# Optimization experiments

Measured on AMD Instinct MI355X. Metric: run time of the kernel, lower is better.

Reference implementation:

```python
import jax, jax.numpy as jnp
import numpy as np

N_NODES = 100000
N_EDGES = 3200000


def gcn_conv(x, edge_index, W, b, num_nodes):
    """PyG GCNConv: x' = D^{-1/2} (A + I) D^{-1/2} (x W) + b (symmetric norm, self-loops)."""
    x = x @ W  # [N, out]
    loop = jnp.arange(num_nodes, dtype=edge_index.dtype)
    src = jnp.concatenate([edge_index[0], loop])
    dst = jnp.concatenate([edge_index[1], loop])
    # degree over destination nodes (incl. self loops)
    deg = jax.ops.segment_sum(jnp.ones_like(dst, dtype=x.dtype), dst, num_segments=num_nodes)
    dinv = jnp.where(deg > 0, jax.lax.rsqrt(deg), 0.0)
    norm = dinv[src] * dinv[dst]  # [E + N]
    msg = x[src] * norm[:, None]  # gather + scale
    out = jax.ops.segment_sum(msg, dst, num_segments=num_nodes)  # scatter-add
    return out + b


def setup_inputs() -> dict:
    key = jax.random.key(0)
    k = jax.random.split(key, 5)
    x = jax.random.normal(k[0], (N_NODES, 256), dtype=jnp.float32)
    edge_index = jax.random.randint(k[1], (2, N_EDGES), 0, N_NODES, dtype=jnp.int64)
    W1 = jax.random.normal(k[2], (256, 16), dtype=jnp.float32) * (1.0 / np.sqrt(256))
    b1 = jnp.zeros((16,), dtype=jnp.float32)
    W2 = jax.random.normal(k[3], (16, 8), dtype=jnp.float32) * (1.0 / np.sqrt(16))
    b2 = jnp.zeros((8,), dtype=jnp.float32)
    return {"x": x, "edge_index": edge_index, "W1": W1, "b1": b1, "W2": W2, "b2": b2}


def reference(x, edge_index, W1, b1, W2, b2):
    n = x.shape[0]
    h = gcn_conv(x, edge_index, W1, b1, n)
    h = jax.nn.relu(h)
    # dropout is identity in eval mode (training=False)
    h = gcn_conv(h, edge_index, W2, b2, n)
    return jax.nn.log_softmax(h, axis=1)
```

## Files before the change

kernel.cpp:

```cpp
#include <hip/hip_runtime.h>

#define NN 100000
#define NE 3200000
#define NB 391
#define CAP 9216
#define PB 16
#define CH_A (256 * PB)
#define BIN_NBLK ((NE + CH_A - 1) / CH_A)
#define GEMM_NBLK (NN / 32)
#define FXS 65536.0f
#define FXI (1.0f / 65536.0f)

typedef _Float16 half4 __attribute__((ext_vector_type(4)));
typedef _Float16 half8 __attribute__((ext_vector_type(8)));

__device__ __forceinline__ float4 f4fma(float s, float4 a, float4 c) {
  c.x = fmaf(s, a.x, c.x); c.y = fmaf(s, a.y, c.y);
  c.z = fmaf(s, a.z, c.z); c.w = fmaf(s, a.w, c.w);
  return c;
}

template<int CTRL>
__device__ __forceinline__ float4 quad_bcast(float4 v) {
  float4 r;
  r.x = __int_as_float(__builtin_amdgcn_update_dpp(__float_as_int(v.x), __float_as_int(v.x), CTRL, 0xF, 0xF, false));
  r.y = __int_as_float(__builtin_amdgcn_update_dpp(__float_as_int(v.y), __float_as_int(v.y), CTRL, 0xF, 0xF, false));
  r.z = __int_as_float(__builtin_amdgcn_update_dpp(__float_as_int(v.z), __float_as_int(v.z), CTRL, 0xF, 0xF, false));
  r.w = __int_as_float(__builtin_amdgcn_update_dpp(__float_as_int(v.w), __float_as_int(v.w), CTRL, 0xF, 0xF, false));
  return r;
}

__global__ __launch_bounds__(256) void k1_kernel(const int* __restrict__ ei,
                                                 int* __restrict__ bucket_cursor,
                                                 int* __restrict__ pairs,
                                                 const float* __restrict__ x,
                                                 const float* __restrict__ W1,
                                                 _Float16* __restrict__ xw1h) {
  int t = threadIdx.x;
  if (blockIdx.x < BIN_NBLK) {
    __shared__ int  cnt[4][NB];
    __shared__ int  wcur[4][NB];
    __shared__ int  lbase[NB];
    __shared__ int  gbase[NB];
    __shared__ int  sc[512];
    __shared__ int2 stage[CH_A];
    __shared__ int  w64flag;
    int wv = t >> 6;
    for (int k = t; k < 4 * NB; k += 256) (&cnt[0][0])[k] = 0;
    if (t < 64) {
      int o = (t < 32) ? ei[2 * t + 1] : 0;
      unsigned long long bl = __ballot(o != 0);
      if (t == 0) w64flag = (bl == 0ULL) ? 1 : 0;
    }
    __syncthreads();
    bool w64 = (w64flag != 0);
    int base = blockIdx.x * CH_A;
    int nval = min(CH_A, NE - base);
    int s[PB], d[PB];
    if (w64) {
#pragma unroll
      for (int i = 0; i < 8; ++i) {
        int e0 = base + i * 512 + 2 * t;
        if (e0 < NE) {
          int4 svv = *(const int4*)(ei + 2 * (size_t)e0);
          int4 dvv = *(const int4*)(ei + 2 * (size_t)NE + 2 * (size_t)e0);
          s[2 * i] = svv.x; s[2 * i + 1] = svv.z;
          d[2 * i] = dvv.x; d[2 * i + 1] = dvv.z;
          atomicAdd(&cnt[wv][dvv.x >> 8], 1);
          atomicAdd(&cnt[wv][dvv.z >> 8], 1);
        } else {
          d[2 * i] = -1; d[2 * i + 1] = -1;
        }
      }
    } else {
#pragma unroll
      for (int i = 0; i < PB; ++i) {
        int e = base + i * 256 + t;
        if (e < NE) {
          s[i] = ei[e];
          d[i] = ei[NE + e];
          atomicAdd(&cnt[wv][d[i] >> 8], 1);
        } else {
          d[i] = -1;
        }
      }
    }
    __syncthreads();
    int tA = (t < NB) ? cnt[0][t] + cnt[1][t] + cnt[2][t] + cnt[3][t] : 0;
    int tB = (t + 256 < NB) ? cnt[0][t + 256] + cnt[1][t + 256] + cnt[2][t + 256] + cnt[3][t + 256] : 0;
    sc[t] = tA; sc[t + 256] = tB;
    __syncthreads();
#pragma unroll
    for (int off = 1; off < 512; off <<= 1) {
      int u0 = (t >= off) ? sc[t - off] : 0;
      int u1 = (t + 256 >= off) ? sc[t + 256 - off] : 0;
      __syncthreads();
      sc[t] += u0; sc[t + 256] += u1;
      __syncthreads();
    }
#pragma unroll
    for (int h = 0; h < 2; ++h) {
      int k = t + h * 256;
      if (k < NB) {
        int tot = (h == 0) ? tA : tB;
        int lb = sc[k] - tot;
        lbase[k] = lb;
        gbase[k] = (tot > 0) ? atomicAdd(&bucket_cursor[k], tot) : 0;
        int c0 = cnt[0][k], c1 = cnt[1][k], c2 = cnt[2][k];
        wcur[0][k] = lb;
        wcur[1][k] = lb + c0;
        wcur[2][k] = lb + c0 + c1;
        wcur[3][k] = lb + c0 + c1 + c2;
      }
    }
    __syncthreads();
#pragma unroll
    for (int i = 0; i < PB; ++i) {
      if (d[i] >= 0) {
        int b = d[i] >> 8;
        int slot = atomicAdd(&wcur[wv][b], 1);
        stage[slot] = make_int2(s[i], d[i]);
      }
    }
    __syncthreads();
    for (int k = t; k < nval; k += 256) {
      int2 p = stage[k];
      int b = p.y >> 8;
      pairs[(size_t)b * CAP + gbase[b] + (k - lbase[b])] = p.x | ((p.y & 255) << 24);
    }
  } else {
    const int bid  = blockIdx.x - BIN_NBLK;
    const int lane = t & 63;
    const int wv   = t >> 6;
    const int node0 = (bid * 4 + wv) * 8;
    const int cg = lane >> 2;
    const int jl = lane & 3;
    float4 w[16];
#pragma unroll
    for (int k = 0; k < 4; ++k)
#pragma unroll
      for (int c = 0; c < 4; ++c)
        w[k * 4 + c] = *(const float4*)(W1 + (cg * 16 + k * 4 + c) * 16 + jl * 4);
    float4 xv[8];
#pragma unroll
    for (int i = 0; i < 8; ++i)
      xv[i] = *(const float4*)(x + (size_t)(node0 + i) * 256 + lane * 4);
    float4 acc[8];
#pragma unroll
    for (int i = 0; i < 8; ++i) acc[i] = make_float4(0.f, 0.f, 0.f, 0.f);
#pragma unroll
    for (int i = 0; i < 8; ++i) {
      float4 b = quad_bcast<0x00>(xv[i]);
      acc[i] = f4fma(b.x, w[0], acc[i]);  acc[i] = f4fma(b.y, w[1], acc[i]);
      acc[i] = f4fma(b.z, w[2], acc[i]);  acc[i] = f4fma(b.w, w[3], acc[i]);
    }
#pragma unroll
    for (int i = 0; i < 8; ++i) {
      float4 b = quad_bcast<0x55>(xv[i]);
      acc[i] = f4fma(b.x, w[4], acc[i]);  acc[i] = f4fma(b.y, w[5], acc[i]);
      acc[i] = f4fma(b.z, w[6], acc[i]);  acc[i] = f4fma(b.w, w[7], acc[i]);
    }
#pragma unroll
    for (int i = 0; i < 8; ++i) {
      float4 b = quad_bcast<0xAA>(xv[i]);
      acc[i] = f4fma(b.x, w[8], acc[i]);  acc[i] = f4fma(b.y, w[9], acc[i]);
      acc[i] = f4fma(b.z, w[10], acc[i]); acc[i] = f4fma(b.w, w[11], acc[i]);
    }
#pragma unroll
    for (int i = 0; i < 8; ++i) {
      float4 b = quad_bcast<0xFF>(xv[i]);
      acc[i] = f4fma(b.x, w[12], acc[i]); acc[i] = f4fma(b.y, w[13], acc[i]);
      acc[i] = f4fma(b.z, w[14], acc[i]); acc[i] = f4fma(b.w, w[15], acc[i]);
    }
#pragma unroll
    for (int m = 4; m <= 32; m <<= 1) {
#pragma unroll
      for (int i = 0; i < 8; ++i) {
        acc[i].x += __shfl_xor(acc[i].x, m);
        acc[i].y += __shfl_xor(acc[i].y, m);
        acc[i].z += __shfl_xor(acc[i].z, m);
        acc[i].w += __shfl_xor(acc[i].w, m);
      }
    }
    if (lane < 4) {
#pragma unroll
      for (int i = 0; i < 8; ++i) {
        float4 a = acc[i];
        half4 hv;
        hv[0] = (_Float16)a.x; hv[1] = (_Float16)a.y;
        hv[2] = (_Float16)a.z; hv[3] = (_Float16)a.w;
        *(half4*)(xw1h + (size_t)(node0 + i) * 16 + lane * 4) = hv;
      }
    }
  }
}

__global__ __launch_bounds__(512) void hist_kernel(const int* __restrict__ pairs,
                                                   const int* __restrict__ bucket_cursor,
                                                   float* __restrict__ dinv) {
  __shared__ int hist[2][256];
  int t = threadIdx.x;
  int b = blockIdx.x;
  int cnt_b = bucket_cursor[b];
  size_t in_base = (size_t)b * CAP;
  if (t < 256) { hist[0][t] = 0; hist[1][t] = 0; }
  __syncthreads();
  int hs = t >> 8;
  for (int i = t; i < cnt_b; i += 512) {
    int pk = pairs[in_base + i];
    atomicAdd(&hist[hs][((unsigned)pk) >> 24], 1);
  }
  __syncthreads();
  if (t < 256) {
    int n = b * 256 + t;
    if (n < NN)
      dinv[n] = rsqrtf((float)(hist[0][t] + hist[1][t]) + 1.0f);
  }
}

__global__ __launch_bounds__(1024) void agg1_kernel(const int* __restrict__ pairs,
                                                    const int* __restrict__ bucket_cursor,
                                                    const float* __restrict__ dinv,
                                                    const _Float16* __restrict__ xw1h,
                                                    const float* __restrict__ W2,
                                                    const float* __restrict__ b1,
                                                    _Float16* __restrict__ h1w2h) {
  __shared__ int acc[16][257];
  int t = threadIdx.x;
  int b = blockIdx.x;
  int cnt_b = bucket_cursor[b];
  size_t in_base = (size_t)b * CAP;
  for (int k = t; k < 16 * 257; k += 1024) (&acc[0][0])[k] = 0;
  __syncthreads();
  for (int i = t; i < cnt_b; i += 1024) {
    int pk = pairs[in_base + i];
    int s  = pk & 0xFFFFFF;
    int nl = ((unsigned)pk) >> 24;
    float dvs = dinv[s] * FXS;
    half8 v0 = *(const half8*)(xw1h + (size_t)s * 16);
    half8 v1 = *(const half8*)(xw1h + (size_t)s * 16 + 8);
#pragma unroll
    for (int j = 0; j < 8; ++j)
      atomicAdd(&acc[j][nl], __float2int_rn((float)v0[j] * dvs));
#pragma unroll
    for (int j = 0; j < 8; ++j)
      atomicAdd(&acc[8 + j][nl], __float2int_rn((float)v1[j] * dvs));
  }
  __syncthreads();
  int n0 = t >> 2, sub = t & 3;
  int n = b * 256 + n0;
  if (n < NN) {
    float dn = dinv[n];
    half4 sv = *(const half4*)(xw1h + (size_t)n * 16 + sub * 4);
    float4 bv = *(const float4*)(b1 + sub * 4);
    float bb[4] = {bv.x, bv.y, bv.z, bv.w};
    float p[8] = {0.f, 0.f, 0.f, 0.f, 0.f, 0.f, 0.f, 0.f};
    const float4* W2v = (const float4*)W2;
#pragma unroll
    for (int f = 0; f < 4; ++f) {
      int fg = sub * 4 + f;
      float aggv = (float)acc[fg][n0] * FXI;
      float h = fmaxf(fmaf(dn, aggv + dn * (float)sv[f], bb[f]), 0.f);
      float4 wlo = W2v[fg * 2];
      float4 whi = W2v[fg * 2 + 1];
      p[0] = fmaf(h, wlo.x, p[0]); p[1] = fmaf(h, wlo.y, p[1]);
      p[2] = fmaf(h, wlo.z, p[2]); p[3] = fmaf(h, wlo.w, p[3]);
      p[4] = fmaf(h, whi.x, p[4]); p[5] = fmaf(h, whi.y, p[5]);
      p[6] = fmaf(h, whi.z, p[6]); p[7] = fmaf(h, whi.w, p[7]);
    }
#pragma unroll
    for (int m = 1; m <= 2; m <<= 1)
#pragma unroll
      for (int j = 0; j < 8; ++j)
        p[j] += __shfl_xor(p[j], m);
    if (sub == 0) {
      half8 hv;
#pragma unroll
      for (int j = 0; j < 8; ++j) hv[j] = (_Float16)(p[j] * dn);
      *(half8*)(h1w2h + (size_t)n * 8) = hv;
    }
  }
}

__global__ __launch_bounds__(1024) void agg2_kernel(const int* __restrict__ pairs,
                                                    const int* __restrict__ bucket_cursor,
                                                    const float* __restrict__ dinv,
                                                    const _Float16* __restrict__ h1w2h,
                                                    const float* __restrict__ b2,
                                                    float* __restrict__ out) {
  __shared__ int acc[8][257];
  int t = threadIdx.x;
  int b = blockIdx.x;
  int cnt_b = bucket_cursor[b];
  size_t in_base = (size_t)b * CAP;
  for (int k = t; k < 8 * 257; k += 1024) (&acc[0][0])[k] = 0;
  __syncthreads();
  for (int i = t; i < cnt_b; i += 1024) {
    int pk = pairs[in_base + i];
    int s  = pk & 0xFFFFFF;
    int nl = ((unsigned)pk) >> 24;
    half8 v = *(const half8*)(h1w2h + (size_t)s * 8);
#pragma unroll
    for (int j = 0; j < 8; ++j)
      atomicAdd(&acc[j][nl], __float2int_rn((float)v[j] * FXS));
  }
  __syncthreads();
  if (t < 512) {
    int n0 = t >> 1, q = t & 1;
    int n = b * 256 + n0;
    if (n < NN) {
      float dn = dinv[n];
      half4 sv = *(const half4*)(h1w2h + (size_t)n * 8 + q * 4);
      float4 bv = *(const float4*)(b2 + q * 4);
      float v0 = fmaf(dn, (float)acc[q * 4 + 0][n0] * FXI + (float)sv[0], bv.x);
      float v1 = fmaf(dn, (float)acc[q * 4 + 1][n0] * FXI + (float)sv[1], bv.y);
      float v2 = fmaf(dn, (float)acc[q * 4 + 2][n0] * FXI + (float)sv[2], bv.z);
      float v3 = fmaf(dn, (float)acc[q * 4 + 3][n0] * FXI + (float)sv[3], bv.w);
      float mh = fmaxf(fmaxf(v0, v1), fmaxf(v2, v3));
      float m = fmaxf(mh, __shfl_xor(mh, 1));
      float se = expf(v0 - m) + expf(v1 - m) + expf(v2 - m) + expf(v3 - m);
      float st = se + __shfl_xor(se, 1);
      float ls = m + logf(st);
      *(float4*)(out + (size_t)n * 8 + q * 4) = make_float4(v0 - ls, v1 - ls, v2 - ls, v3 - ls);
    }
  }
}

extern "C" void kernel_launch(void* const* d_in, const int* in_sizes, int n_in,
                              void* d_out, int out_size, void* d_ws, size_t ws_size,
                              hipStream_t stream) {
  const float* x  = (const float*)d_in[0];
  const int*   ei = (const int*)d_in[1];
  const float* W1 = (const float*)d_in[2];
  const float* b1 = (const float*)d_in[3];
  const float* W2 = (const float*)d_in[4];
  const float* b2 = (const float*)d_in[5];
  float* out = (float*)d_out;

  float*    dinv          = (float*)d_ws;
  int*      bucket_cursor = (int*)(dinv + NN);
  int*      pairs         = (int*)dinv + 100400;
  _Float16* xw1h  = (_Float16*)(pairs + (size_t)NB * CAP);
  _Float16* h1w2h = xw1h + (size_t)16 * NN;

  hipMemsetAsync(bucket_cursor, 0, (size_t)NB * sizeof(int), stream);
  k1_kernel<<<BIN_NBLK + GEMM_NBLK, 256, 0, stream>>>(ei, bucket_cursor, pairs, x, W1, xw1h);
  hist_kernel<<<NB, 512, 0, stream>>>(pairs, bucket_cursor, dinv);
  agg1_kernel<<<NB, 1024, 0, stream>>>(pairs, bucket_cursor, dinv, xw1h, W2, b1, h1w2h);
  agg2_kernel<<<NB, 1024, 0, stream>>>(pairs, bucket_cursor, dinv, h1w2h, b2, out);
}
```

Baseline: 287.6 us.

## Fuse degree, both aggregations into one persistent kernel with grid barriers

Replaces the three per-bucket kernels (histogram, layer-1 aggregation, layer-2 aggregation) with one kernel that uses a software grid barrier between phases. Buckets grow from 256 to 512 destination nodes, which halves the block count so all 196 blocks can be co-resident. The packed pair format changes to a 17-bit source and 9-bit local index, and dinv is kept in LDS for local nodes. This removes two kernel launches and their tails, but relies on every block being resident for the spin barrier. It also leaves fewer, larger blocks on the GPU and raises LDS atomic traffic per block.

```diff
diff --git a/kernel.cpp b/kernel.cpp
--- a/kernel.cpp
+++ b/kernel.cpp
@@ -2,12 +2,13 @@
 
 #define NN 100000
 #define NE 3200000
-#define NB 391
-#define CAP 9216
+#define NB 196
+#define CAP 17664
 #define PB 16
 #define CH_A (256 * PB)
 #define BIN_NBLK ((NE + CH_A - 1) / CH_A)
 #define GEMM_NBLK (NN / 32)
+#define SMASK 0x1FFFF
 #define FXS 65536.0f
 #define FXI (1.0f / 65536.0f)
 
@@ -28,6 +29,18 @@
   r.z = __int_as_float(__builtin_amdgcn_update_dpp(__float_as_int(v.z), __float_as_int(v.z), CTRL, 0xF, 0xF, false));
   r.w = __int_as_float(__builtin_amdgcn_update_dpp(__float_as_int(v.w), __float_as_int(v.w), CTRL, 0xF, 0xF, false));
   return r;
+}
+
+__device__ __forceinline__ void gbar(int* bar, int target) {
+  __syncthreads();
+  __threadfence();
+  if (threadIdx.x == 0) {
+    atomicAdd(bar, 1);
+    while (atomicAdd(bar, 0) < target)
+      __builtin_amdgcn_s_sleep(2);
+    __threadfence();
+  }
+  __syncthreads();
 }
 
 __global__ __launch_bounds__(256) void k1_kernel(const int* __restrict__ ei,
@@ -42,7 +55,7 @@
     __shared__ int  wcur[4][NB];
     __shared__ int  lbase[NB];
     __shared__ int  gbase[NB];
-    __shared__ int  sc[512];
+    __shared__ int  sc[256];
     __shared__ int2 stage[CH_A];
     __shared__ int  w64flag;
     int wv = t >> 6;
@@ -66,8 +79,8 @@
           int4 dvv = *(const int4*)(ei + 2 * (size_t)NE + 2 * (size_t)e0);
           s[2 * i] = svv.x; s[2 * i + 1] = svv.z;
           d[2 * i] = dvv.x; d[2 * i + 1] = dvv.z;
-          atomicAdd(&cnt[wv][dvv.x >> 8], 1);
-          atomicAdd(&cnt[wv][dvv.z >> 8], 1);
+          atomicAdd(&cnt[wv][dvv.x >> 9], 1);
+          atomicAdd(&cnt[wv][dvv.z >> 9], 1);
         } else {
           d[2 * i] = -1; d[2 * i + 1] = -1;
         }
@@ -79,7 +92,7 @@
         if (e < NE) {
           s[i] = ei[e];
           d[i] = ei[NE + e];
-          atomicAdd(&cnt[wv][d[i] >> 8], 1);
+          atomicAdd(&cnt[wv][d[i] >> 9], 1);
         } else {
           d[i] = -1;
         }
@@ -87,37 +100,30 @@
     }
     __syncthreads();
     int tA = (t < NB) ? cnt[0][t] + cnt[1][t] + cnt[2][t] + cnt[3][t] : 0;
-    int tB = (t + 256 < NB) ? cnt[0][t + 256] + cnt[1][t + 256] + cnt[2][t + 256] + cnt[3][t + 256] : 0;
-    sc[t] = tA; sc[t + 256] = tB;
-    __syncthreads();
-#pragma unroll
-    for (int off = 1; off < 512; off <<= 1) {
-      int u0 = (t >= off) ? sc[t - off] : 0;
-      int u1 = (t + 256 >= off) ? sc[t + 256 - off] : 0;
+    sc[t] = tA;
+    __syncthreads();
+#pragma unroll
+    for (int off = 1; off < 256; off <<= 1) {
+      int u = (t >= off) ? sc[t - off] : 0;
       __syncthreads();
-      sc[t] += u0; sc[t + 256] += u1;
+      sc[t] += u;
       __syncthreads();
     }
-#pragma unroll
-    for (int h = 0; h < 2; ++h) {
-      int k = t + h * 256;
-      if (k < NB) {
-        int tot = (h == 0) ? tA : tB;
-        int lb = sc[k] - tot;
-        lbase[k] = lb;
-        gbase[k] = (tot > 0) ? atomicAdd(&bucket_cursor[k], tot) : 0;
-        int c0 = cnt[0][k], c1 = cnt[1][k], c2 = cnt[2][k];
-        wcur[0][k] = lb;
-        wcur[1][k] = lb + c0;
-        wcur[2][k] = lb + c0 + c1;
-        wcur[3][k] = lb + c0 + c1 + c2;
-      }
+    if (t < NB) {
+      int lb = sc[t] - tA;
+      lbase[t] = lb;
+      gbase[t] = (tA > 0) ? atomicAdd(&bucket_cursor[t], tA) : 0;
+      int c0 = cnt[0][t], c1 = cnt[1][t], c2 = cnt[2][t];
+      wcur[0][t] = lb;
+      wcur[1][t] = lb + c0;
+      wcur[2][t] = lb + c0 + c1;
+      wcur[3][t] = lb + c0 + c1 + c2;
     }
     __syncthreads();
 #pragma unroll
     for (int i = 0; i < PB; ++i) {
       if (d[i] >= 0) {
-        int b = d[i] >> 8;
+        int b = d[i] >> 9;
         int slot = atomicAdd(&wcur[wv][b], 1);
         stage[slot] = make_int2(s[i], d[i]);
       }
@@ -125,22 +131,22 @@
     __syncthreads();
     for (int k = t; k < nval; k += 256) {
       int2 p = stage[k];
-      int b = p.y >> 8;
-      pairs[(size_t)b * CAP + gbase[b] + (k - lbase[b])] = p.x | ((p.y & 255) << 24);
+      int b = p.y >> 9;
+      pairs[(size_t)b * CAP + gbase[b] + (k - lbase[b])] = p.x | ((p.y & 511) << 17);
     }
   } else {
     const int bid  = blockIdx.x - BIN_NBLK;
     const int lane = t & 63;
     const int wv   = t >> 6;
     const int node0 = (bid * 4 + wv) * 8;
-    const int cg = lane >> 2;
+    const int cg_ = lane >> 2;
     const int jl = lane & 3;
     float4 w[16];
 #pragma unroll
     for (int k = 0; k < 4; ++k)
 #pragma unroll
       for (int c = 0; c < 4; ++c)
-        w[k * 4 + c] = *(const float4*)(W1 + (cg * 16 + k * 4 + c) * 16 + jl * 4);
+        w[k * 4 + c] = *(const float4*)(W1 + (cg_ * 16 + k * 4 + c) * 16 + jl * 4);
     float4 xv[8];
 #pragma unroll
     for (int i = 0; i < 8; ++i)
@@ -195,121 +201,112 @@
   }
 }
 
-__global__ __launch_bounds__(512) void hist_kernel(const int* __restrict__ pairs,
-                                                   const int* __restrict__ bucket_cursor,
-                                                   float* __restrict__ dinv) {
-  __shared__ int hist[2][256];
+__global__ __launch_bounds__(1024, 4) void k2_kernel(const int* __restrict__ pairs,
+                                                     const int* __restrict__ bucket_cursor,
+                                                     const _Float16* __restrict__ xw1h,
+                                                     const float* __restrict__ W2,
+                                                     const float* __restrict__ b1,
+                                                     const float* __restrict__ b2,
+                                                     float* __restrict__ dinv,
+                                                     _Float16* __restrict__ h1w2h,
+                                                     float* __restrict__ out,
+                                                     int* __restrict__ bar) {
+  __shared__ int   acc[16][512];
+  __shared__ int   hist2[2][512];
+  __shared__ float dlds[512];
   int t = threadIdx.x;
   int b = blockIdx.x;
   int cnt_b = bucket_cursor[b];
   size_t in_base = (size_t)b * CAP;
-  if (t < 256) { hist[0][t] = 0; hist[1][t] = 0; }
-  __syncthreads();
-  int hs = t >> 8;
-  for (int i = t; i < cnt_b; i += 512) {
-    int pk = pairs[in_base + i];
-    atomicAdd(&hist[hs][((unsigned)pk) >> 24], 1);
-  }
-  __syncthreads();
-  if (t < 256) {
-    int n = b * 256 + t;
-    if (n < NN)
-      dinv[n] = rsqrtf((float)(hist[0][t] + hist[1][t]) + 1.0f);
-  }
-}
-
-__global__ __launch_bounds__(1024) void agg1_kernel(const int* __restrict__ pairs,
-                                                    const int* __restrict__ bucket_cursor,
-                                                    const float* __restrict__ dinv,
-                                                    const _Float16* __restrict__ xw1h,
-                                                    const float* __restrict__ W2,
-                                                    const float* __restrict__ b1,
-                                                    _Float16* __restrict__ h1w2h) {
-  __shared__ int acc[16][257];
-  int t = threadIdx.x;
-  int b = blockIdx.x;
-  int cnt_b = bucket_cursor[b];
-  size_t in_base = (size_t)b * CAP;
-  for (int k = t; k < 16 * 257; k += 1024) (&acc[0][0])[k] = 0;
-  __syncthreads();
+
+  ((int*)hist2)[t] = 0;
+  __syncthreads();
+  int hs = t >> 9;
   for (int i = t; i < cnt_b; i += 1024) {
     int pk = pairs[in_base + i];
-    int s  = pk & 0xFFFFFF;
-    int nl = ((unsigned)pk) >> 24;
+    atomicAdd(&hist2[hs][((unsigned)pk) >> 17], 1);
+  }
+  __syncthreads();
+  if (t < 512) {
+    int n = b * 512 + t;
+    if (n < NN) {
+      float dv = rsqrtf((float)(hist2[0][t] + hist2[1][t]) + 1.0f);
+      dinv[n] = dv;
+      dlds[t] = dv;
+    }
+  }
+  gbar(bar, NB);
+
+  for (int k = t; k < 16 * 512; k += 1024) (&acc[0][0])[k] = 0;
+  __syncthreads();
+  for (int i = t; i < cnt_b; i += 1024) {
+    int pk = pairs[in_base + i];
+    int s  = pk & SMASK;
+    int nl = ((unsigned)pk) >> 17;
     float dvs = dinv[s] * FXS;
     half8 v0 = *(const half8*)(xw1h + (size_t)s * 16);
     half8 v1 = *(const half8*)(xw1h + (size_t)s * 16 + 8);
 #pragma unroll
-    for (int j = 0; j < 8; ++j)
-      atomicAdd(&acc[j][nl], __float2int_rn((float)v0[j] * dvs));
-#pragma unroll
-    for (int j = 0; j < 8; ++j)
-      atomicAdd(&acc[8 + j][nl], __float2int_rn((float)v1[j] * dvs));
-  }
-  __syncthreads();
-  int n0 = t >> 2, sub = t & 3;
-  int n = b * 256 + n0;
-  if (n < NN) {
-    float dn = dinv[n];
-    half4 sv = *(const half4*)(xw1h + (size_t)n * 16 + sub * 4);
-    float4 bv = *(const float4*)(b1 + sub * 4);
-    float bb[4] = {bv.x, bv.y, bv.z, bv.w};
-    float p[8] = {0.f, 0.f, 0.f, 0.f, 0.f, 0.f, 0.f, 0.f};
-    const float4* W2v = (const float4*)W2;
-#pragma unroll
-    for (int f = 0; f < 4; ++f) {
-      int fg = sub * 4 + f;
-      float aggv = (float)acc[fg][n0] * FXI;
-      float h = fmaxf(fmaf(dn, aggv + dn * (float)sv[f], bb[f]), 0.f);
-      float4 wlo = W2v[fg * 2];
-      float4 whi = W2v[fg * 2 + 1];
-      p[0] = fmaf(h, wlo.x, p[0]); p[1] = fmaf(h, wlo.y, p[1]);
-      p[2] = fmaf(h, wlo.z, p[2]); p[3] = fmaf(h, wlo.w, p[3]);
-      p[4] = fmaf(h, whi.x, p[4]); p[5] = fmaf(h, whi.y, p[5]);
-      p[6] = fmaf(h, whi.z, p[6]); p[7] = fmaf(h, whi.w, p[7]);
-    }
-#pragma unroll
-    for (int m = 1; m <= 2; m <<= 1)
-#pragma unroll
-      for (int j = 0; j < 8; ++j)
-        p[j] += __shfl_xor(p[j], m);
-    if (sub == 0) {
-      half8 hv;
-#pragma unroll
-      for (int j = 0; j < 8; ++j) hv[j] = (_Float16)(p[j] * dn);
-      *(half8*)(h1w2h + (size_t)n * 8) = hv;
-    }
-  }
-}
-
-__global__ __launch_bounds__(1024) void agg2_kernel(const int* __restrict__ pairs,
-                                                    const int* __restrict__ bucket_cursor,
-                                                    const float* __restrict__ dinv,
-                                                    const _Float16* __restrict__ h1w2h,
-                                                    const float* __restrict__ b2,
-                                                    float* __restrict__ out) {
-  __shared__ int acc[8][257];
-  int t = threadIdx.x;
-  int b = blockIdx.x;
-  int cnt_b = bucket_cursor[b];
-  size_t in_base = (size_t)b * CAP;
-  for (int k = t; k < 8 * 257; k += 1024) (&acc[0][0])[k] = 0;
+    for (int f = 0; f < 8; ++f)
+      atomicAdd(&acc[f][nl], __float2int_rn((float)v0[f] * dvs));
+#pragma unroll
+    for (int f = 0; f < 8; ++f)
+      atomicAdd(&acc[8 + f][nl], __float2int_rn((float)v1[f] * dvs));
+  }
+  __syncthreads();
+  {
+    int n0 = t >> 1, sub = t & 1;
+    int n = b * 512 + n0;
+    if (n < NN) {
+      float dn = dlds[n0];
+      half8 sv = *(const half8*)(xw1h + (size_t)n * 16 + sub * 8);
+      float4 blo = *(const float4*)(b1 + sub * 8);
+      float4 bhi = *(const float4*)(b1 + sub * 8 + 4);
+      float bb[8] = {blo.x, blo.y, blo.z, blo.w, bhi.x, bhi.y, bhi.z, bhi.w};
+      float p[8] = {0.f, 0.f, 0.f, 0.f, 0.f, 0.f, 0.f, 0.f};
+      const float4* W2v = (const float4*)W2;
+#pragma unroll
+      for (int f = 0; f < 8; ++f) {
+        int fg = sub * 8 + f;
+        float aggv = (float)acc[fg][n0] * FXI;
+        float h = fmaxf(fmaf(dn, aggv + dn * (float)sv[f], bb[f]), 0.f);
+        float4 wlo = W2v[fg * 2];
+        float4 whi = W2v[fg * 2 + 1];
+        p[0] = fmaf(h, wlo.x, p[0]); p[1] = fmaf(h, wlo.y, p[1]);
+        p[2] = fmaf(h, wlo.z, p[2]); p[3] = fmaf(h, wlo.w, p[3]);
+        p[4] = fmaf(h, whi.x, p[4]); p[5] = fmaf(h, whi.y, p[5]);
+        p[6] = fmaf(h, whi.z, p[6]); p[7] = fmaf(h, whi.w, p[7]);
+      }
+#pragma unroll
+      for (int jj = 0; jj < 8; ++jj)
+        p[jj] += __shfl_xor(p[jj], 1);
+      if (sub == 0) {
+        half8 hv;
+#pragma unroll
+        for (int jj = 0; jj < 8; ++jj) hv[jj] = (_Float16)(p[jj] * dn);
+        *(half8*)(h1w2h + (size_t)n * 8) = hv;
+      }
+    }
+  }
+  gbar(bar, 2 * NB);
+
+  for (int k = t; k < 8 * 512; k += 1024) (&acc[0][0])[k] = 0;
   __syncthreads();
   for (int i = t; i < cnt_b; i += 1024) {
     int pk = pairs[in_base + i];
-    int s  = pk & 0xFFFFFF;
-    int nl = ((unsigned)pk) >> 24;
+    int s  = pk & SMASK;
+    int nl = ((unsigned)pk) >> 17;
     half8 v = *(const half8*)(h1w2h + (size_t)s * 8);
 #pragma unroll
-    for (int j = 0; j < 8; ++j)
-      atomicAdd(&acc[j][nl], __float2int_rn((float)v[j] * FXS));
-  }
-  __syncthreads();
-  if (t < 512) {
+    for (int f = 0; f < 8; ++f)
+      atomicAdd(&acc[f][nl], __float2int_rn((float)v[f] * FXS));
+  }
+  __syncthreads();
+  {
     int n0 = t >> 1, q = t & 1;
-    int n = b * 256 + n0;
+    int n = b * 512 + n0;
     if (n < NN) {
-      float dn = dinv[n];
+      float dn = dlds[n0];
       half4 sv = *(const half4*)(h1w2h + (size_t)n * 8 + q * 4);
       float4 bv = *(const float4*)(b2 + q * 4);
       float v0 = fmaf(dn, (float)acc[q * 4 + 0][n0] * FXI + (float)sv[0], bv.x);
@@ -339,13 +336,13 @@
 
   float*    dinv          = (float*)d_ws;
   int*      bucket_cursor = (int*)(dinv + NN);
+  int*      bar           = bucket_cursor + NB;
   int*      pairs         = (int*)dinv + 100400;
   _Float16* xw1h  = (_Float16*)(pairs + (size_t)NB * CAP);
   _Float16* h1w2h = xw1h + (size_t)16 * NN;
 
-  hipMemsetAsync(bucket_cursor, 0, (size_t)NB * sizeof(int), stream);
+  hipMemsetAsync(bucket_cursor, 0, (size_t)(NB + 1) * sizeof(int), stream);
   k1_kernel<<<BIN_NBLK + GEMM_NBLK, 256, 0, stream>>>(ei, bucket_cursor, pairs, x, W1, xw1h);
-  hist_kernel<<<NB, 512, 0, stream>>>(pairs, bucket_cursor, dinv);
-  agg1_kernel<<<NB, 1024, 0, stream>>>(pairs, bucket_cursor, dinv, xw1h, W2, b1, h1w2h);
-  agg2_kernel<<<NB, 1024, 0, stream>>>(pairs, bucket_cursor, dinv, h1w2h, b2, out);
-}
+  k2_kernel<<<NB, 1024, 0, stream>>>(pairs, bucket_cursor, xw1h, W2, b1, b2,
+                                     dinv, h1w2h, out, bar);
+}
```

After: 382.1 us. +32.8%, slower.

## Prescale xw1h by dinv in hist kernel and split agg gathers across thread pairs

Applied to the files above, without the earlier changes.

The hist kernel now multiplies each node's xw1h row by its dinv once, so agg1 no longer gathers dinv[s] per edge and the self-loop term drops one multiply. agg1 assigns two threads per edge, each loading half of the 16-feature row, which gives more parallel gather traffic. Both aggregation loops software-prefetch the next packed pair index. This adds a read-modify-write pass over xw1h and an extra fp16 rounding step after scaling.

```diff
diff --git a/kernel.cpp b/kernel.cpp
--- a/kernel.cpp
+++ b/kernel.cpp
@@ -133,14 +133,14 @@
     const int lane = t & 63;
     const int wv   = t >> 6;
     const int node0 = (bid * 4 + wv) * 8;
-    const int cg = lane >> 2;
+    const int cg_ = lane >> 2;
     const int jl = lane & 3;
     float4 w[16];
 #pragma unroll
     for (int k = 0; k < 4; ++k)
 #pragma unroll
       for (int c = 0; c < 4; ++c)
-        w[k * 4 + c] = *(const float4*)(W1 + (cg * 16 + k * 4 + c) * 16 + jl * 4);
+        w[k * 4 + c] = *(const float4*)(W1 + (cg_ * 16 + k * 4 + c) * 16 + jl * 4);
     float4 xv[8];
 #pragma unroll
     for (int i = 0; i < 8; ++i)
@@ -197,8 +197,10 @@
 
 __global__ __launch_bounds__(512) void hist_kernel(const int* __restrict__ pairs,
                                                    const int* __restrict__ bucket_cursor,
-                                                   float* __restrict__ dinv) {
+                                                   float* __restrict__ dinv,
+                                                   _Float16* __restrict__ xw1h) {
   __shared__ int hist[2][256];
+  __shared__ float dl[256];
   int t = threadIdx.x;
   int b = blockIdx.x;
   int cnt_b = bucket_cursor[b];
@@ -213,8 +215,24 @@
   __syncthreads();
   if (t < 256) {
     int n = b * 256 + t;
-    if (n < NN)
-      dinv[n] = rsqrtf((float)(hist[0][t] + hist[1][t]) + 1.0f);
+    if (n < NN) {
+      float dv = rsqrtf((float)(hist[0][t] + hist[1][t]) + 1.0f);
+      dinv[n] = dv;
+      dl[t] = dv;
+    }
+  }
+  __syncthreads();
+  {
+    int n0 = t >> 1, h = t & 1;
+    int n = b * 256 + n0;
+    if (n < NN) {
+      float dv = dl[n0];
+      half8* p8 = (half8*)(xw1h + (size_t)n * 16 + h * 8);
+      half8 v = *p8;
+#pragma unroll
+      for (int f = 0; f < 8; ++f) v[f] = (_Float16)((float)v[f] * dv);
+      *p8 = v;
+    }
   }
 }
 
@@ -232,19 +250,20 @@
   size_t in_base = (size_t)b * CAP;
   for (int k = t; k < 16 * 257; k += 1024) (&acc[0][0])[k] = 0;
   __syncthreads();
-  for (int i = t; i < cnt_b; i += 1024) {
-    int pk = pairs[in_base + i];
-    int s  = pk & 0xFFFFFF;
-    int nl = ((unsigned)pk) >> 24;
-    float dvs = dinv[s] * FXS;
-    half8 v0 = *(const half8*)(xw1h + (size_t)s * 16);
-    half8 v1 = *(const half8*)(xw1h + (size_t)s * 16 + 8);
-#pragma unroll
-    for (int j = 0; j < 8; ++j)
-      atomicAdd(&acc[j][nl], __float2int_rn((float)v0[j] * dvs));
-#pragma unroll
-    for (int j = 0; j < 8; ++j)
-      atomicAdd(&acc[8 + j][nl], __float2int_rn((float)v1[j] * dvs));
+  {
+    int hh = t & 1;
+    int i = t >> 1;
+    int pkn = (i < cnt_b) ? pairs[in_base + i] : 0;
+    for (; i < cnt_b; i += 512) {
+      int pk = pkn;
+      if (i + 512 < cnt_b) pkn = pairs[in_base + i + 512];
+      int s  = pk & 0xFFFFFF;
+      int nl = ((unsigned)pk) >> 24;
+      half8 v = *(const half8*)(xw1h + (size_t)s * 16 + hh * 8);
+#pragma unroll
+      for (int f = 0; f < 8; ++f)
+        atomicAdd(&acc[hh * 8 + f][nl], __float2int_rn((float)v[f] * FXS));
+    }
   }
   __syncthreads();
   int n0 = t >> 2, sub = t & 3;
@@ -260,7 +279,7 @@
     for (int f = 0; f < 4; ++f) {
       int fg = sub * 4 + f;
       float aggv = (float)acc[fg][n0] * FXI;
-      float h = fmaxf(fmaf(dn, aggv + dn * (float)sv[f], bb[f]), 0.f);
+      float h = fmaxf(fmaf(dn, aggv + (float)sv[f], bb[f]), 0.f);
       float4 wlo = W2v[fg * 2];
       float4 whi = W2v[fg * 2 + 1];
       p[0] = fmaf(h, wlo.x, p[0]); p[1] = fmaf(h, wlo.y, p[1]);
@@ -295,14 +314,19 @@
   size_t in_base = (size_t)b * CAP;
   for (int k = t; k < 8 * 257; k += 1024) (&acc[0][0])[k] = 0;
   __syncthreads();
-  for (int i = t; i < cnt_b; i += 1024) {
-    int pk = pairs[in_base + i];
-    int s  = pk & 0xFFFFFF;
-    int nl = ((unsigned)pk) >> 24;
-    half8 v = *(const half8*)(h1w2h + (size_t)s * 8);
-#pragma unroll
-    for (int j = 0; j < 8; ++j)
-      atomicAdd(&acc[j][nl], __float2int_rn((float)v[j] * FXS));
+  {
+    int i = t;
+    int pkn = (i < cnt_b) ? pairs[in_base + i] : 0;
+    for (; i < cnt_b; i += 1024) {
+      int pk = pkn;
+      if (i + 1024 < cnt_b) pkn = pairs[in_base + i + 1024];
+      int s  = pk & 0xFFFFFF;
+      int nl = ((unsigned)pk) >> 24;
+      half8 v = *(const half8*)(h1w2h + (size_t)s * 8);
+#pragma unroll
+      for (int j = 0; j < 8; ++j)
+        atomicAdd(&acc[j][nl], __float2int_rn((float)v[j] * FXS));
+    }
   }
   __syncthreads();
   if (t < 512) {
@@ -345,7 +369,7 @@
 
   hipMemsetAsync(bucket_cursor, 0, (size_t)NB * sizeof(int), stream);
   k1_kernel<<<BIN_NBLK + GEMM_NBLK, 256, 0, stream>>>(ei, bucket_cursor, pairs, x, W1, xw1h);
-  hist_kernel<<<NB, 512, 0, stream>>>(pairs, bucket_cursor, dinv);
+  hist_kernel<<<NB, 512, 0, stream>>>(pairs, bucket_cursor, dinv, xw1h);
   agg1_kernel<<<NB, 1024, 0, stream>>>(pairs, bucket_cursor, dinv, xw1h, W2, b1, h1w2h);
   agg2_kernel<<<NB, 1024, 0, stream>>>(pairs, bucket_cursor, dinv, h1w2h, b2, out);
 }
```

After: 268.4 us. 1.07x faster.
